# Performance work log

Measured on AMD Instinct MI355X. Metric: run time of the kernel, lower is better.

## Reference

```python
import jax, jax.numpy as jnp
import numpy as np

B, T, D = 4, 2048, 1024
H = 16
HD = D // H

def setup_inputs() -> dict:
    key = jax.random.key(0)
    k1, k2, k3, k4, k5 = jax.random.split(key, 5)
    x = jax.random.normal(k1, (B, T, D), dtype=jnp.float32)
    scale = 1.0 / np.sqrt(D)
    W_qkv = jax.random.normal(k2, (D, 3 * D), dtype=jnp.float32) * scale
    b_qkv = jnp.zeros((3 * D,), dtype=jnp.float32)
    W_proj = jax.random.normal(k3, (D, D), dtype=jnp.float32) * scale
    b_proj = jnp.zeros((D,), dtype=jnp.float32)
    return {"x": x, "W_qkv": W_qkv, "b_qkv": b_qkv, "W_proj": W_proj, "b_proj": b_proj}

def reference(x, W_qkv, b_qkv, W_proj, b_proj):
    Bx, Tx, C = x.shape
    qkv = x @ W_qkv + b_qkv                      # [B,T,3C]
    q, k, v = jnp.split(qkv, 3, axis=-1)
    # [B,T,H,hd] -> [B,H,T,hd]
    q = q.reshape(Bx, Tx, H, HD).transpose(0, 2, 1, 3)
    k = k.reshape(Bx, Tx, H, HD).transpose(0, 2, 1, 3)
    v = v.reshape(Bx, Tx, H, HD).transpose(0, 2, 1, 3)
    att = jnp.einsum('bhqd,bhkd->bhqk', q, k) / jnp.sqrt(jnp.float32(HD))
    causal = jnp.tril(jnp.ones((Tx, Tx), dtype=bool))
    att = jnp.where(causal[None, None], att, -jnp.inf)
    att = jax.nn.softmax(att, axis=-1)
    y = jnp.einsum('bhqk,bhkd->bhqd', att, v)    # [B,H,T,hd]
    y = y.transpose(0, 2, 1, 3).reshape(Bx, Tx, C)
    return y @ W_proj + b_proj
```

## Files before the change

### kernel.cpp

```cpp
#include <hip/hip_runtime.h>
#include <hip/hip_bf16.h>

#define B_  4
#define T_  2048
#define D_  1024
#define H_  16
#define HD_ 64

typedef short s16x8 __attribute__((ext_vector_type(8)));
typedef short s16x4 __attribute__((ext_vector_type(4)));
typedef float f32x4 __attribute__((ext_vector_type(4)));
typedef unsigned int u32x2 __attribute__((ext_vector_type(2)));

#define MFMA32(a, b, c) __builtin_amdgcn_mfma_f32_16x16x32_bf16(a, b, c, 0, 0, 0)
#define MFMA16(a, b, c) __builtin_amdgcn_mfma_f32_16x16x16bf16_1k(a, b, c, 0, 0, 0)

__device__ __forceinline__ unsigned short f2bf(float f) {
  unsigned u = __builtin_bit_cast(unsigned, f);
  u += 0x7fffu + ((u >> 16) & 1u);
  return (unsigned short)(u >> 16);
}

__device__ __forceinline__ float bf2f(unsigned short h) {
  return __builtin_bit_cast(float, (unsigned)h << 16);
}

#define GLOAD_LDS16(src, dst)                                            \
  __builtin_amdgcn_global_load_lds(                                      \
      (__attribute__((address_space(1))) void*)(void*)(src),             \
      (__attribute__((address_space(3))) void*)(dst), 16, 0, 0)

__global__ __launch_bounds__(256) void convert_x_kernel(
    const float* __restrict__ in, unsigned short* __restrict__ out, int n8) {
  int i = blockIdx.x * 256 + threadIdx.x;
  if (i >= n8) return;
  const float4* p = ((const float4*)in) + (size_t)i * 2;
  float4 a = p[0], b = p[1];
  s16x8 o;
  o[0] = (short)f2bf(a.x); o[1] = (short)f2bf(a.y);
  o[2] = (short)f2bf(a.z); o[3] = (short)f2bf(a.w);
  o[4] = (short)f2bf(b.x); o[5] = (short)f2bf(b.y);
  o[6] = (short)f2bf(b.z); o[7] = (short)f2bf(b.w);
  *(((s16x8*)out) + i) = o;
}

__global__ __launch_bounds__(256) void transpose_w_kernel(
    const float* __restrict__ W, unsigned short* __restrict__ Wt, int K, int N) {
  __shared__ float tile[32][33];
  int n0 = blockIdx.x * 32, k0 = blockIdx.y * 32;
  int tx = threadIdx.x & 31, ty = threadIdx.x >> 5;
#pragma unroll
  for (int j = 0; j < 4; ++j) {
    int k = ty + j * 8;
    tile[k][tx] = W[(size_t)(k0 + k) * N + n0 + tx];
  }
  __syncthreads();
#pragma unroll
  for (int j = 0; j < 4; ++j) {
    int n = ty + j * 8;
    Wt[(size_t)(n0 + n) * K + k0 + tx] = f2bf(tile[tx][n]);
  }
}

template <int OUTF32>
__global__ __launch_bounds__(256) void gemm_kernel(
    const unsigned short* __restrict__ A, const unsigned short* __restrict__ Bt,
    const float* __restrict__ bias, void* __restrict__ Cout, int M, int N, int K) {
  __shared__ char lds[32768];
  char* Al = lds;
  char* Bl = lds + 16384;
  const int n0 = blockIdx.x * 128, m0 = blockIdx.y * 128;
  const int w = threadIdx.x >> 6, lane = threadIdx.x & 63;
  const int l15 = lane & 15, g = lane >> 4;
  const int wr = w >> 1, wc = w & 1;
  const int srow = (lane >> 3);
  const int u = lane & 7;
  const int soct = (u ^ srow) << 3;
  const int rx = l15 & 7;
  f32x4 acc[4][4] = {};

  for (int kt = 0; kt < K; kt += 64) {
    __syncthreads();
#pragma unroll
    for (int i = 0; i < 4; ++i) {
      int c = w * 4 + i;
      int row = c * 8 + srow;
      const unsigned short* srcA = A + (size_t)(m0 + row) * K + kt + soct;
      GLOAD_LDS16(srcA, Al + c * 1024);
      const unsigned short* srcB = Bt + (size_t)(n0 + row) * K + kt + soct;
      GLOAD_LDS16(srcB, Bl + c * 1024);
    }
    __syncthreads();
#pragma unroll
    for (int kk = 0; kk < 2; ++kk) {
      const int roct = ((kk * 4 + g) ^ rx) << 4;
      s16x8 af[4], bfr[4];
#pragma unroll
      for (int mi = 0; mi < 4; ++mi) {
        int row = wr * 64 + mi * 16 + l15;
        af[mi] = *(const s16x8*)(Al + row * 128 + roct);
      }
#pragma unroll
      for (int ni = 0; ni < 4; ++ni) {
        int row = wc * 64 + ni * 16 + l15;
        bfr[ni] = *(const s16x8*)(Bl + row * 128 + roct);
      }
#pragma unroll
      for (int mi = 0; mi < 4; ++mi)
#pragma unroll
        for (int ni = 0; ni < 4; ++ni)
          acc[mi][ni] = MFMA32(af[mi], bfr[ni], acc[mi][ni]);
    }
  }
#pragma unroll
  for (int ni = 0; ni < 4; ++ni) {
    int col = n0 + wc * 64 + ni * 16 + l15;
    float bv = bias[col];
#pragma unroll
    for (int mi = 0; mi < 4; ++mi) {
      int row = m0 + wr * 64 + mi * 16 + g * 4;
#pragma unroll
      for (int r = 0; r < 4; ++r) {
        float v = acc[mi][ni][r] + bv;
        if (OUTF32)
          ((float*)Cout)[(size_t)(row + r) * N + col] = v;
        else
          ((unsigned short*)Cout)[(size_t)(row + r) * N + col] = f2bf(v);
      }
    }
  }
}

#define VT_STR 76
#define VT_BLK 1232
__global__ __launch_bounds__(256, 2) void attn_kernel(
    const unsigned short* __restrict__ qkv, unsigned short* __restrict__ yatt) {
  __shared__ char lds[18048];
  const int bx = blockIdx.x;
  const int bh = blockIdx.y;
  const int b = bh >> 4, h = bh & 15;
  const int w = threadIdx.x >> 6;
  const int lane = threadIdx.x & 63;
  const int l15 = lane & 15, g = lane >> 4;

  const size_t rowstride = 3 * D_;
  const unsigned short* Qb = qkv + (size_t)b * T_ * rowstride + h * HD_;
  const unsigned short* Kb = Qb + D_;
  const unsigned short* Vb = Qb + 2 * D_;

  char* Klds = lds;
  unsigned short* Vt = (unsigned short*)(lds + 8192);

  const int krow0 = (w * 2 + 0) * 8 + (lane >> 3);
  const int krow1 = (w * 2 + 1) * 8 + (lane >> 3);
  const int u = lane & 7;
  const int vkey = w * 16 + (lane >> 2);
  const int vdb = lane & 3;
  const float SC = 0.18033688011112042f;
  const s16x4 onesf = {(short)0x3F80, (short)0x3F80, (short)0x3F80, (short)0x3F80};

  const int qtA_t = 15 - bx;
  const int nA = 2 * qtA_t + 2;

  s16x8 kc0, kc1, vc0, vc1;
  s16x8 kn0, kn1, vn0, vn1;

  auto ld = [&](int kt, s16x8& a, s16x8& b2, s16x8& c, s16x8& d2) {
    const unsigned short* kb = Kb + (size_t)(kt * 64) * rowstride;
    a = *(const s16x8*)(kb + (size_t)krow0 * rowstride + u * 8);
    b2 = *(const s16x8*)(kb + (size_t)krow1 * rowstride + u * 8);
    const unsigned short* vs = Vb + (size_t)(kt * 64 + vkey) * rowstride + vdb * 16;
    c = *(const s16x8*)(vs);
    d2 = *(const s16x8*)(vs + 8);
  };

  ld(0, kc0, kc1, vc0, vc1);
  ld(1, kn0, kn1, vn0, vn1);
  int f = 0;

#pragma unroll 1
  for (int ti = 0; ti < 2; ++ti) {
    const int qt = ti ? bx : qtA_t;
    const int ntk = 2 * qt + 2;
    const int base = qt * 128 + w * 32;
    s16x8 qfA0, qfA1, qfB0, qfB1;
    {
      const unsigned short* qa = Qb + (size_t)(base + l15) * rowstride;
      const unsigned short* qb = Qb + (size_t)(base + 16 + l15) * rowstride;
      s16x8 a0 = *(const s16x8*)(qa + g * 8);
      s16x8 a1 = *(const s16x8*)(qa + 32 + g * 8);
      s16x8 b0 = *(const s16x8*)(qb + g * 8);
      s16x8 b1 = *(const s16x8*)(qb + 32 + g * 8);
#pragma unroll
      for (int j = 0; j < 8; ++j) {
        qfA0[j] = (short)f2bf(bf2f((unsigned short)a0[j]) * SC);
        qfA1[j] = (short)f2bf(bf2f((unsigned short)a1[j]) * SC);
        qfB0[j] = (short)f2bf(bf2f((unsigned short)b0[j]) * SC);
        qfB1[j] = (short)f2bf(bf2f((unsigned short)b1[j]) * SC);
      }
    }
    float mA = -1e30f, mB = -1e30f;
    f32x4 accA[4] = {}, accB[4] = {};
    f32x4 accSA = {}, accSB = {};

#pragma unroll 1
    for (int kt = 0; kt < ntk; ++kt) {
      __syncthreads();
      *(s16x8*)(Klds + krow0 * 128 + ((u ^ (krow0 & 7)) << 4)) = kc0;
      *(s16x8*)(Klds + krow1 * 128 + ((u ^ (krow1 & 7)) << 4)) = kc1;
#pragma unroll
      for (int j = 0; j < 8; ++j) {
        Vt[vdb * VT_BLK + j * VT_STR + vkey] = (unsigned short)vc0[j];
        Vt[vdb * VT_BLK + (8 + j) * VT_STR + vkey] = (unsigned short)vc1[j];
      }
      __syncthreads();
      kc0 = kn0; kc1 = kn1; vc0 = vn0; vc1 = vn1;
      {
        int f2 = f + 2;
        if (f2 < 34) {
          int kt2 = (f2 < nA) ? f2 : f2 - nA;
          ld(kt2, kn0, kn1, vn0, vn1);
        }
      }
      ++f;

      if (kt * 64 > base + 31) continue;

      float tvA[16], tvB[16];
      __builtin_amdgcn_s_setprio(1);
#pragma unroll
      for (int kk = 0; kk < 4; ++kk) {
        int key = kk * 16 + l15;
        const s16x8 kf0 = *(const s16x8*)(Klds + key * 128 + ((g ^ (key & 7)) << 4));
        const s16x8 kf1 = *(const s16x8*)(Klds + key * 128 + (((4 + g) ^ (key & 7)) << 4));
        f32x4 sA = {}, sB = {};
        sA = MFMA32(kf0, qfA0, sA);
        sA = MFMA32(kf1, qfA1, sA);
        sB = MFMA32(kf0, qfB0, sB);
        sB = MFMA32(kf1, qfB1, sB);
#pragma unroll
        for (int r = 0; r < 4; ++r) { tvA[kk * 4 + r] = sA[r]; tvB[kk * 4 + r] = sB[r]; }
      }
      __builtin_amdgcn_s_setprio(0);
      if (kt * 64 + 63 > base) {
        int qA = base + l15, qB = base + 16 + l15;
#pragma unroll
        for (int kk = 0; kk < 4; ++kk)
#pragma unroll
          for (int r = 0; r < 4; ++r) {
            int key = kt * 64 + kk * 16 + g * 4 + r;
            if (key > qA) tvA[kk * 4 + r] = -1e30f;
            if (key > qB) tvB[kk * 4 + r] = -1e30f;
          }
      }
      s16x4 pbA[4], pbB[4];
      {
        float a0 = fmaxf(fmaxf(tvA[0], tvA[1]), tvA[2]);
        float a1 = fmaxf(fmaxf(tvA[3], tvA[4]), tvA[5]);
        float a2 = fmaxf(fmaxf(tvA[6], tvA[7]), tvA[8]);
        float a3 = fmaxf(fmaxf(tvA[9], tvA[10]), tvA[11]);
        float a4 = fmaxf(fmaxf(tvA[12], tvA[13]), tvA[14]);
        float tm = fmaxf(fmaxf(fmaxf(a0, a1), a2), fmaxf(fmaxf(a3, a4), tvA[15]));
        tm = fmaxf(tm, __shfl_xor(tm, 16));
        tm = fmaxf(tm, __shfl_xor(tm, 32));
        if (!__all(tm - mA <= 8.0f)) {
          float mn = fmaxf(mA, tm);
          float corr = exp2f(mA - mn);
          mA = mn;
#pragma unroll
          for (int i = 0; i < 4; ++i) {
            accA[i][0] *= corr; accA[i][1] *= corr;
            accA[i][2] *= corr; accA[i][3] *= corr;
          }
          accSA[0] *= corr; accSA[1] *= corr; accSA[2] *= corr; accSA[3] *= corr;
        }
#pragma unroll
        for (int kk = 0; kk < 4; ++kk) {
          float p0 = exp2f(tvA[kk * 4 + 0] - mA), p1 = exp2f(tvA[kk * 4 + 1] - mA);
          float p2 = exp2f(tvA[kk * 4 + 2] - mA), p3 = exp2f(tvA[kk * 4 + 3] - mA);
          u32x2 pk;
          pk[0] = __builtin_amdgcn_perm(__builtin_bit_cast(unsigned, p1),
                                        __builtin_bit_cast(unsigned, p0), 0x07060302u);
          pk[1] = __builtin_amdgcn_perm(__builtin_bit_cast(unsigned, p3),
                                        __builtin_bit_cast(unsigned, p2), 0x07060302u);
          pbA[kk] = __builtin_bit_cast(s16x4, pk);
        }
      }
      {
        float a0 = fmaxf(fmaxf(tvB[0], tvB[1]), tvB[2]);
        float a1 = fmaxf(fmaxf(tvB[3], tvB[4]), tvB[5]);
        float a2 = fmaxf(fmaxf(tvB[6], tvB[7]), tvB[8]);
        float a3 = fmaxf(fmaxf(tvB[9], tvB[10]), tvB[11]);
        float a4 = fmaxf(fmaxf(tvB[12], tvB[13]), tvB[14]);
        float tm = fmaxf(fmaxf(fmaxf(a0, a1), a2), fmaxf(fmaxf(a3, a4), tvB[15]));
        tm = fmaxf(tm, __shfl_xor(tm, 16));
        tm = fmaxf(tm, __shfl_xor(tm, 32));
        if (!__all(tm - mB <= 8.0f)) {
          float mn = fmaxf(mB, tm);
          float corr = exp2f(mB - mn);
          mB = mn;
#pragma unroll
          for (int i = 0; i < 4; ++i) {
            accB[i][0] *= corr; accB[i][1] *= corr;
            accB[i][2] *= corr; accB[i][3] *= corr;
          }
          accSB[0] *= corr; accSB[1] *= corr; accSB[2] *= corr; accSB[3] *= corr;
        }
#pragma unroll
        for (int kk = 0; kk < 4; ++kk) {
          float p0 = exp2f(tvB[kk * 4 + 0] - mB), p1 = exp2f(tvB[kk * 4 + 1] - mB);
          float p2 = exp2f(tvB[kk * 4 + 2] - mB), p3 = exp2f(tvB[kk * 4 + 3] - mB);
          u32x2 pk;
          pk[0] = __builtin_amdgcn_perm(__builtin_bit_cast(unsigned, p1),
                                        __builtin_bit_cast(unsigned, p0), 0x07060302u);
          pk[1] = __builtin_amdgcn_perm(__builtin_bit_cast(unsigned, p3),
                                        __builtin_bit_cast(unsigned, p2), 0x07060302u);
          pbB[kk] = __builtin_bit_cast(s16x4, pk);
        }
      }
      __builtin_amdgcn_s_setprio(1);
#pragma unroll
      for (int kk = 0; kk < 4; ++kk) {
#pragma unroll
        for (int db = 0; db < 4; ++db) {
          s16x4 vf = *(const s16x4*)(Vt + db * VT_BLK + l15 * VT_STR + kk * 16 + g * 4);
          accA[db] = MFMA16(vf, pbA[kk], accA[db]);
          accB[db] = MFMA16(vf, pbB[kk], accB[db]);
        }
        accSA = MFMA16(onesf, pbA[kk], accSA);
        accSB = MFMA16(onesf, pbB[kk], accSB);
      }
      __builtin_amdgcn_s_setprio(0);
    }

    float invA = 1.0f / accSA[0];
    float invB = 1.0f / accSB[0];
    __syncthreads();
    unsigned short* ylds = (unsigned short*)lds;
#pragma unroll
    for (int db = 0; db < 4; ++db)
#pragma unroll
      for (int r = 0; r < 4; ++r) {
        int d = db * 16 + g * 4 + r;
        ylds[d * 130 + w * 32 + l15] = f2bf(accA[db][r] * invA);
        ylds[d * 130 + w * 32 + 16 + l15] = f2bf(accB[db][r] * invB);
      }
    __syncthreads();
    {
      int qq = threadIdx.x >> 1;
      int dc = (threadIdx.x & 1) * 32;
      s16x8 o0, o1, o2, o3;
#pragma unroll
      for (int j = 0; j < 8; ++j) {
        o0[j] = (short)ylds[(dc + j) * 130 + qq];
        o1[j] = (short)ylds[(dc + 8 + j) * 130 + qq];
        o2[j] = (short)ylds[(dc + 16 + j) * 130 + qq];
        o3[j] = (short)ylds[(dc + 24 + j) * 130 + qq];
      }
      unsigned short* dst =
          yatt + (size_t)(b * T_ + qt * 128 + qq) * D_ + h * HD_ + dc;
      *(s16x8*)(dst) = o0;
      *(s16x8*)(dst + 8) = o1;
      *(s16x8*)(dst + 16) = o2;
      *(s16x8*)(dst + 24) = o3;
    }
  }
}

extern "C" void kernel_launch(void* const* d_in, const int* in_sizes, int n_in,
                              void* d_out, int out_size, void* d_ws, size_t ws_size,
                              hipStream_t stream) {
  const float* x     = (const float*)d_in[0];
  const float* Wqkv  = (const float*)d_in[1];
  const float* bqkv  = (const float*)d_in[2];
  const float* Wproj = (const float*)d_in[3];
  const float* bproj = (const float*)d_in[4];
  float* out = (float*)d_out;

  unsigned short* xb   = (unsigned short*)d_ws;
  unsigned short* Wqb  = xb + (size_t)8192 * 1024;
  unsigned short* Wpb  = Wqb + (size_t)3072 * 1024;
  unsigned short* qkvb = Wpb + (size_t)1024 * 1024;
  unsigned short* yb   = xb;

  convert_x_kernel<<<dim3(4096), dim3(256), 0, stream>>>(x, xb, 8192 * 1024 / 8);
  transpose_w_kernel<<<dim3(96, 32), dim3(256), 0, stream>>>(Wqkv, Wqb, 1024, 3072);
  transpose_w_kernel<<<dim3(32, 32), dim3(256), 0, stream>>>(Wproj, Wpb, 1024, 1024);
  gemm_kernel<0><<<dim3(24, 64), dim3(256), 0, stream>>>(xb, Wqb, bqkv, qkvb, 8192, 3072, 1024);
  attn_kernel<<<dim3(8, 64), dim3(256), 0, stream>>>(qkvb, yb);
  gemm_kernel<1><<<dim3(8, 64), dim3(256), 0, stream>>>(yb, Wpb, bproj, out, 8192, 1024, 1024);
}
```

Measured before the change: 193.2 us.

## Double-buffer GEMM LDS loads and split attention into one query tile per block

After: 185.1 us. 4.2% less time.

```diff
diff --git a/kernel.cpp b/kernel.cpp
--- a/kernel.cpp
+++ b/kernel.cpp
@@ -63,12 +63,10 @@
 }
 
 template <int OUTF32>
-__global__ __launch_bounds__(256) void gemm_kernel(
+__global__ __launch_bounds__(256, 2) void gemm_kernel(
     const unsigned short* __restrict__ A, const unsigned short* __restrict__ Bt,
     const float* __restrict__ bias, void* __restrict__ Cout, int M, int N, int K) {
-  __shared__ char lds[32768];
-  char* Al = lds;
-  char* Bl = lds + 16384;
+  __shared__ char lds[65536];
   const int n0 = blockIdx.x * 128, m0 = blockIdx.y * 128;
   const int w = threadIdx.x >> 6, lane = threadIdx.x & 63;
   const int l15 = lane & 15, g = lane >> 4;
@@ -79,18 +77,34 @@
   const int rx = l15 & 7;
   f32x4 acc[4][4] = {};
 
-  for (int kt = 0; kt < K; kt += 64) {
-    __syncthreads();
+  auto stage = [&](int buf, int kt) {
+    char* Ab = lds + buf * 32768;
+    char* Bb = Ab + 16384;
 #pragma unroll
     for (int i = 0; i < 4; ++i) {
       int c = w * 4 + i;
       int row = c * 8 + srow;
-      const unsigned short* srcA = A + (size_t)(m0 + row) * K + kt + soct;
-      GLOAD_LDS16(srcA, Al + c * 1024);
-      const unsigned short* srcB = Bt + (size_t)(n0 + row) * K + kt + soct;
-      GLOAD_LDS16(srcB, Bl + c * 1024);
-    }
-    __syncthreads();
+      GLOAD_LDS16(A + (size_t)(m0 + row) * K + kt + soct, Ab + c * 1024);
+      GLOAD_LDS16(Bt + (size_t)(n0 + row) * K + kt + soct, Bb + c * 1024);
+    }
+  };
+
+  stage(0, 0);
+  __syncthreads();
+  int cur = 0;
+
+  for (int kt = 0; kt < K; kt += 64) {
+    __builtin_amdgcn_s_barrier();
+    if (kt + 64 < K) {
+      stage(cur ^ 1, kt + 64);
+      asm volatile("s_waitcnt vmcnt(8)" ::: "memory");
+    } else {
+      asm volatile("s_waitcnt vmcnt(0)" ::: "memory");
+    }
+    __builtin_amdgcn_s_barrier();
+    __builtin_amdgcn_sched_barrier(0);
+    const char* Al = lds + cur * 32768;
+    const char* Bl = Al + 16384;
 #pragma unroll
     for (int kk = 0; kk < 2; ++kk) {
       const int roct = ((kk * 4 + g) ^ rx) << 4;
@@ -111,6 +125,7 @@
         for (int ni = 0; ni < 4; ++ni)
           acc[mi][ni] = MFMA32(af[mi], bfr[ni], acc[mi][ni]);
     }
+    cur ^= 1;
   }
 #pragma unroll
   for (int ni = 0; ni < 4; ++ni) {
@@ -133,11 +148,11 @@
 
 #define VT_STR 76
 #define VT_BLK 1232
-__global__ __launch_bounds__(256, 2) void attn_kernel(
+__global__ __launch_bounds__(256, 4) void attn_kernel(
     const unsigned short* __restrict__ qkv, unsigned short* __restrict__ yatt) {
-  __shared__ char lds[18048];
-  const int bx = blockIdx.x;
-  const int bh = blockIdx.y;
+  __shared__ char lds[8192 + 4 * VT_BLK * 2];
+  const int bh = blockIdx.x;
+  const int qt = 15 - blockIdx.y;
   const int b = bh >> 4, h = bh & 15;
   const int w = threadIdx.x >> 6;
   const int lane = threadIdx.x & 63;
@@ -159,211 +174,193 @@
   const float SC = 0.18033688011112042f;
   const s16x4 onesf = {(short)0x3F80, (short)0x3F80, (short)0x3F80, (short)0x3F80};
 
-  const int qtA_t = 15 - bx;
-  const int nA = 2 * qtA_t + 2;
-
-  s16x8 kc0, kc1, vc0, vc1;
-  s16x8 kn0, kn1, vn0, vn1;
-
-  auto ld = [&](int kt, s16x8& a, s16x8& b2, s16x8& c, s16x8& d2) {
+  s16x8 kreg0, kreg1, vreg0, vreg1;
+  auto ld = [&](int kt) {
     const unsigned short* kb = Kb + (size_t)(kt * 64) * rowstride;
-    a = *(const s16x8*)(kb + (size_t)krow0 * rowstride + u * 8);
-    b2 = *(const s16x8*)(kb + (size_t)krow1 * rowstride + u * 8);
+    kreg0 = *(const s16x8*)(kb + (size_t)krow0 * rowstride + u * 8);
+    kreg1 = *(const s16x8*)(kb + (size_t)krow1 * rowstride + u * 8);
     const unsigned short* vs = Vb + (size_t)(kt * 64 + vkey) * rowstride + vdb * 16;
-    c = *(const s16x8*)(vs);
-    d2 = *(const s16x8*)(vs + 8);
+    vreg0 = *(const s16x8*)(vs);
+    vreg1 = *(const s16x8*)(vs + 8);
   };
 
-  ld(0, kc0, kc1, vc0, vc1);
-  ld(1, kn0, kn1, vn0, vn1);
-  int f = 0;
+  const int base = qt * 128 + w * 32;
+  const int ntk = 2 * qt + 2;
+
+  s16x8 qfA0, qfA1, qfB0, qfB1;
+  {
+    const unsigned short* qa = Qb + (size_t)(base + l15) * rowstride;
+    const unsigned short* qb = Qb + (size_t)(base + 16 + l15) * rowstride;
+    s16x8 a0 = *(const s16x8*)(qa + g * 8);
+    s16x8 a1 = *(const s16x8*)(qa + 32 + g * 8);
+    s16x8 b0 = *(const s16x8*)(qb + g * 8);
+    s16x8 b1 = *(const s16x8*)(qb + 32 + g * 8);
+#pragma unroll
+    for (int j = 0; j < 8; ++j) {
+      qfA0[j] = (short)f2bf(bf2f((unsigned short)a0[j]) * SC);
+      qfA1[j] = (short)f2bf(bf2f((unsigned short)a1[j]) * SC);
+      qfB0[j] = (short)f2bf(bf2f((unsigned short)b0[j]) * SC);
+      qfB1[j] = (short)f2bf(bf2f((unsigned short)b1[j]) * SC);
+    }
+  }
+
+  ld(0);
+  float mA = -1e30f, mB = -1e30f;
+  f32x4 accA[4] = {}, accB[4] = {};
+  f32x4 accSA = {}, accSB = {};
 
 #pragma unroll 1
-  for (int ti = 0; ti < 2; ++ti) {
-    const int qt = ti ? bx : qtA_t;
-    const int ntk = 2 * qt + 2;
-    const int base = qt * 128 + w * 32;
-    s16x8 qfA0, qfA1, qfB0, qfB1;
+  for (int kt = 0; kt < ntk; ++kt) {
+    __syncthreads();
+    *(s16x8*)(Klds + krow0 * 128 + ((u ^ (krow0 & 7)) << 4)) = kreg0;
+    *(s16x8*)(Klds + krow1 * 128 + ((u ^ (krow1 & 7)) << 4)) = kreg1;
+#pragma unroll
+    for (int j = 0; j < 8; ++j) {
+      Vt[vdb * VT_BLK + j * VT_STR + vkey] = (unsigned short)vreg0[j];
+      Vt[vdb * VT_BLK + (8 + j) * VT_STR + vkey] = (unsigned short)vreg1[j];
+    }
+    __syncthreads();
+    if (kt < ntk - 1) ld(kt + 1);
+
+    if (kt * 64 > base + 31) continue;
+
+    float tvA[16], tvB[16];
+    __builtin_amdgcn_s_setprio(1);
+#pragma unroll
+    for (int kk = 0; kk < 4; ++kk) {
+      int key = kk * 16 + l15;
+      const s16x8 kf0 = *(const s16x8*)(Klds + key * 128 + ((g ^ (key & 7)) << 4));
+      const s16x8 kf1 = *(const s16x8*)(Klds + key * 128 + (((4 + g) ^ (key & 7)) << 4));
+      f32x4 sA = {}, sB = {};
+      sA = MFMA32(kf0, qfA0, sA);
+      sA = MFMA32(kf1, qfA1, sA);
+      sB = MFMA32(kf0, qfB0, sB);
+      sB = MFMA32(kf1, qfB1, sB);
+#pragma unroll
+      for (int r = 0; r < 4; ++r) { tvA[kk * 4 + r] = sA[r]; tvB[kk * 4 + r] = sB[r]; }
+    }
+    __builtin_amdgcn_s_setprio(0);
+    if (kt * 64 + 63 > base) {
+      int qA = base + l15, qB = base + 16 + l15;
+#pragma unroll
+      for (int kk = 0; kk < 4; ++kk)
+#pragma unroll
+        for (int r = 0; r < 4; ++r) {
+          int key = kt * 64 + kk * 16 + g * 4 + r;
+          if (key > qA) tvA[kk * 4 + r] = -1e30f;
+          if (key > qB) tvB[kk * 4 + r] = -1e30f;
+        }
+    }
+    s16x4 pbA[4], pbB[4];
     {
-      const unsigned short* qa = Qb + (size_t)(base + l15) * rowstride;
-      const unsigned short* qb = Qb + (size_t)(base + 16 + l15) * rowstride;
-      s16x8 a0 = *(const s16x8*)(qa + g * 8);
-      s16x8 a1 = *(const s16x8*)(qa + 32 + g * 8);
-      s16x8 b0 = *(const s16x8*)(qb + g * 8);
-      s16x8 b1 = *(const s16x8*)(qb + 32 + g * 8);
-#pragma unroll
-      for (int j = 0; j < 8; ++j) {
-        qfA0[j] = (short)f2bf(bf2f((unsigned short)a0[j]) * SC);
-        qfA1[j] = (short)f2bf(bf2f((unsigned short)a1[j]) * SC);
-        qfB0[j] = (short)f2bf(bf2f((unsigned short)b0[j]) * SC);
-        qfB1[j] = (short)f2bf(bf2f((unsigned short)b1[j]) * SC);
-      }
-    }
-    float mA = -1e30f, mB = -1e30f;
-    f32x4 accA[4] = {}, accB[4] = {};
-    f32x4 accSA = {}, accSB = {};
-
-#pragma unroll 1
-    for (int kt = 0; kt < ntk; ++kt) {
-      __syncthreads();
-      *(s16x8*)(Klds + krow0 * 128 + ((u ^ (krow0 & 7)) << 4)) = kc0;
-      *(s16x8*)(Klds + krow1 * 128 + ((u ^ (krow1 & 7)) << 4)) = kc1;
-#pragma unroll
-      for (int j = 0; j < 8; ++j) {
-        Vt[vdb * VT_BLK + j * VT_STR + vkey] = (unsigned short)vc0[j];
-        Vt[vdb * VT_BLK + (8 + j) * VT_STR + vkey] = (unsigned short)vc1[j];
-      }
-      __syncthreads();
-      kc0 = kn0; kc1 = kn1; vc0 = vn0; vc1 = vn1;
-      {
-        int f2 = f + 2;
-        if (f2 < 34) {
-          int kt2 = (f2 < nA) ? f2 : f2 - nA;
-          ld(kt2, kn0, kn1, vn0, vn1);
+      float a0 = fmaxf(fmaxf(tvA[0], tvA[1]), tvA[2]);
+      float a1 = fmaxf(fmaxf(tvA[3], tvA[4]), tvA[5]);
+      float a2 = fmaxf(fmaxf(tvA[6], tvA[7]), tvA[8]);
+      float a3 = fmaxf(fmaxf(tvA[9], tvA[10]), tvA[11]);
+      float a4 = fmaxf(fmaxf(tvA[12], tvA[13]), tvA[14]);
+      float tm = fmaxf(fmaxf(fmaxf(a0, a1), a2), fmaxf(fmaxf(a3, a4), tvA[15]));
+      tm = fmaxf(tm, __shfl_xor(tm, 16));
+      tm = fmaxf(tm, __shfl_xor(tm, 32));
+      if (!__all(tm - mA <= 8.0f)) {
+        float mn = fmaxf(mA, tm);
+        float corr = exp2f(mA - mn);
+        mA = mn;
+#pragma unroll
+        for (int i = 0; i < 4; ++i) {
+          accA[i][0] *= corr; accA[i][1] *= corr;
+          accA[i][2] *= corr; accA[i][3] *= corr;
         }
-      }
-      ++f;
-
-      if (kt * 64 > base + 31) continue;
-
-      float tvA[16], tvB[16];
-      __builtin_amdgcn_s_setprio(1);
+        accSA[0] *= corr; accSA[1] *= corr; accSA[2] *= corr; accSA[3] *= corr;
+      }
 #pragma unroll
       for (int kk = 0; kk < 4; ++kk) {
-        int key = kk * 16 + l15;
-        const s16x8 kf0 = *(const s16x8*)(Klds + key * 128 + ((g ^ (key & 7)) << 4));
-        const s16x8 kf1 = *(const s16x8*)(Klds + key * 128 + (((4 + g) ^ (key & 7)) << 4));
-        f32x4 sA = {}, sB = {};
-        sA = MFMA32(kf0, qfA0, sA);
-        sA = MFMA32(kf1, qfA1, sA);
-        sB = MFMA32(kf0, qfB0, sB);
-        sB = MFMA32(kf1, qfB1, sB);
-#pragma unroll
-        for (int r = 0; r < 4; ++r) { tvA[kk * 4 + r] = sA[r]; tvB[kk * 4 + r] = sB[r]; }
-      }
-      __builtin_amdgcn_s_setprio(0);
-      if (kt * 64 + 63 > base) {
-        int qA = base + l15, qB = base + 16 + l15;
-#pragma unroll
-        for (int kk = 0; kk < 4; ++kk)
-#pragma unroll
-          for (int r = 0; r < 4; ++r) {
-            int key = kt * 64 + kk * 16 + g * 4 + r;
-            if (key > qA) tvA[kk * 4 + r] = -1e30f;
-            if (key > qB) tvB[kk * 4 + r] = -1e30f;
-          }
-      }
-      s16x4 pbA[4], pbB[4];
-      {
-        float a0 = fmaxf(fmaxf(tvA[0], tvA[1]), tvA[2]);
-        float a1 = fmaxf(fmaxf(tvA[3], tvA[4]), tvA[5]);
-        float a2 = fmaxf(fmaxf(tvA[6], tvA[7]), tvA[8]);
-        float a3 = fmaxf(fmaxf(tvA[9], tvA[10]), tvA[11]);
-        float a4 = fmaxf(fmaxf(tvA[12], tvA[13]), tvA[14]);
-        float tm = fmaxf(fmaxf(fmaxf(a0, a1), a2), fmaxf(fmaxf(a3, a4), tvA[15]));
-        tm = fmaxf(tm, __shfl_xor(tm, 16));
-        tm = fmaxf(tm, __shfl_xor(tm, 32));
-        if (!__all(tm - mA <= 8.0f)) {
-          float mn = fmaxf(mA, tm);
-          float corr = exp2f(mA - mn);
-          mA = mn;
-#pragma unroll
-          for (int i = 0; i < 4; ++i) {
-            accA[i][0] *= corr; accA[i][1] *= corr;
-            accA[i][2] *= corr; accA[i][3] *= corr;
-          }
-          accSA[0] *= corr; accSA[1] *= corr; accSA[2] *= corr; accSA[3] *= corr;
+        float p0 = exp2f(tvA[kk * 4 + 0] - mA), p1 = exp2f(tvA[kk * 4 + 1] - mA);
+        float p2 = exp2f(tvA[kk * 4 + 2] - mA), p3 = exp2f(tvA[kk * 4 + 3] - mA);
+        u32x2 pk;
+        pk[0] = __builtin_amdgcn_perm(__builtin_bit_cast(unsigned, p1),
+                                      __builtin_bit_cast(unsigned, p0), 0x07060302u);
+        pk[1] = __builtin_amdgcn_perm(__builtin_bit_cast(unsigned, p3),
+                                      __builtin_bit_cast(unsigned, p2), 0x07060302u);
+        pbA[kk] = __builtin_bit_cast(s16x4, pk);
+      }
+    }
+    {
+      float a0 = fmaxf(fmaxf(tvB[0], tvB[1]), tvB[2]);
+      float a1 = fmaxf(fmaxf(tvB[3], tvB[4]), tvB[5]);
+      float a2 = fmaxf(fmaxf(tvB[6], tvB[7]), tvB[8]);
+      float a3 = fmaxf(fmaxf(tvB[9], tvB[10]), tvB[11]);
+      float a4 = fmaxf(fmaxf(tvB[12], tvB[13]), tvB[14]);
+      float tm = fmaxf(fmaxf(fmaxf(a0, a1), a2), fmaxf(fmaxf(a3, a4), tvB[15]));
+      tm = fmaxf(tm, __shfl_xor(tm, 16));
+      tm = fmaxf(tm, __shfl_xor(tm, 32));
+      if (!__all(tm - mB <= 8.0f)) {
+        float mn = fmaxf(mB, tm);
+        float corr = exp2f(mB - mn);
+        mB = mn;
+#pragma unroll
+        for (int i = 0; i < 4; ++i) {
+          accB[i][0] *= corr; accB[i][1] *= corr;
+          accB[i][2] *= corr; accB[i][3] *= corr;
         }
-#pragma unroll
-        for (int kk = 0; kk < 4; ++kk) {
-          float p0 = exp2f(tvA[kk * 4 + 0] - mA), p1 = exp2f(tvA[kk * 4 + 1] - mA);
-          float p2 = exp2f(tvA[kk * 4 + 2] - mA), p3 = exp2f(tvA[kk * 4 + 3] - mA);
-          u32x2 pk;
-          pk[0] = __builtin_amdgcn_perm(__builtin_bit_cast(unsigned, p1),
-                                        __builtin_bit_cast(unsigned, p0), 0x07060302u);
-          pk[1] = __builtin_amdgcn_perm(__builtin_bit_cast(unsigned, p3),
-                                        __builtin_bit_cast(unsigned, p2), 0x07060302u);
-          pbA[kk] = __builtin_bit_cast(s16x4, pk);
-        }
-      }
-      {
-        float a0 = fmaxf(fmaxf(tvB[0], tvB[1]), tvB[2]);
-        float a1 = fmaxf(fmaxf(tvB[3], tvB[4]), tvB[5]);
-        float a2 = fmaxf(fmaxf(tvB[6], tvB[7]), tvB[8]);
-        float a3 = fmaxf(fmaxf(tvB[9], tvB[10]), tvB[11]);
-        float a4 = fmaxf(fmaxf(tvB[12], tvB[13]), tvB[14]);
-        float tm = fmaxf(fmaxf(fmaxf(a0, a1), a2), fmaxf(fmaxf(a3, a4), tvB[15]));
-        tm = fmaxf(tm, __shfl_xor(tm, 16));
-        tm = fmaxf(tm, __shfl_xor(tm, 32));
-        if (!__all(tm - mB <= 8.0f)) {
-          float mn = fmaxf(mB, tm);
-          float corr = exp2f(mB - mn);
-          mB = mn;
-#pragma unroll
-          for (int i = 0; i < 4; ++i) {
-            accB[i][0] *= corr; accB[i][1] *= corr;
-            accB[i][2] *= corr; accB[i][3] *= corr;
-          }
-          accSB[0] *= corr; accSB[1] *= corr; accSB[2] *= corr; accSB[3] *= corr;
-        }
-#pragma unroll
-        for (int kk = 0; kk < 4; ++kk) {
-          float p0 = exp2f(tvB[kk * 4 + 0] - mB), p1 = exp2f(tvB[kk * 4 + 1] - mB);
-          float p2 = exp2f(tvB[kk * 4 + 2] - mB), p3 = exp2f(tvB[kk * 4 + 3] - mB);
-          u32x2 pk;
-          pk[0] = __builtin_amdgcn_perm(__builtin_bit_cast(unsigned, p1),
-                                        __builtin_bit_cast(unsigned, p0), 0x07060302u);
-          pk[1] = __builtin_amdgcn_perm(__builtin_bit_cast(unsigned, p3),
-                                        __builtin_bit_cast(unsigned, p2), 0x07060302u);
-          pbB[kk] = __builtin_bit_cast(s16x4, pk);
-        }
-      }
-      __builtin_amdgcn_s_setprio(1);
+        accSB[0] *= corr; accSB[1] *= corr; accSB[2] *= corr; accSB[3] *= corr;
+      }
 #pragma unroll
       for (int kk = 0; kk < 4; ++kk) {
-#pragma unroll
-        for (int db = 0; db < 4; ++db) {
-          s16x4 vf = *(const s16x4*)(Vt + db * VT_BLK + l15 * VT_STR + kk * 16 + g * 4);
-          accA[db] = MFMA16(vf, pbA[kk], accA[db]);
-          accB[db] = MFMA16(vf, pbB[kk], accB[db]);
-        }
-        accSA = MFMA16(onesf, pbA[kk], accSA);
-        accSB = MFMA16(onesf, pbB[kk], accSB);
-      }
-      __builtin_amdgcn_s_setprio(0);
-    }
-
-    float invA = 1.0f / accSA[0];
-    float invB = 1.0f / accSB[0];
-    __syncthreads();
-    unsigned short* ylds = (unsigned short*)lds;
-#pragma unroll
-    for (int db = 0; db < 4; ++db)
-#pragma unroll
-      for (int r = 0; r < 4; ++r) {
-        int d = db * 16 + g * 4 + r;
-        ylds[d * 130 + w * 32 + l15] = f2bf(accA[db][r] * invA);
-        ylds[d * 130 + w * 32 + 16 + l15] = f2bf(accB[db][r] * invB);
-      }
-    __syncthreads();
-    {
-      int qq = threadIdx.x >> 1;
-      int dc = (threadIdx.x & 1) * 32;
-      s16x8 o0, o1, o2, o3;
-#pragma unroll
-      for (int j = 0; j < 8; ++j) {
-        o0[j] = (short)ylds[(dc + j) * 130 + qq];
-        o1[j] = (short)ylds[(dc + 8 + j) * 130 + qq];
-        o2[j] = (short)ylds[(dc + 16 + j) * 130 + qq];
-        o3[j] = (short)ylds[(dc + 24 + j) * 130 + qq];
-      }
-      unsigned short* dst =
-          yatt + (size_t)(b * T_ + qt * 128 + qq) * D_ + h * HD_ + dc;
-      *(s16x8*)(dst) = o0;
-      *(s16x8*)(dst + 8) = o1;
-      *(s16x8*)(dst + 16) = o2;
-      *(s16x8*)(dst + 24) = o3;
-    }
+        float p0 = exp2f(tvB[kk * 4 + 0] - mB), p1 = exp2f(tvB[kk * 4 + 1] - mB);
+        float p2 = exp2f(tvB[kk * 4 + 2] - mB), p3 = exp2f(tvB[kk * 4 + 3] - mB);
+        u32x2 pk;
+        pk[0] = __builtin_amdgcn_perm(__builtin_bit_cast(unsigned, p1),
+                                      __builtin_bit_cast(unsigned, p0), 0x07060302u);
+        pk[1] = __builtin_amdgcn_perm(__builtin_bit_cast(unsigned, p3),
+                                      __builtin_bit_cast(unsigned, p2), 0x07060302u);
+        pbB[kk] = __builtin_bit_cast(s16x4, pk);
+      }
+    }
+    __builtin_amdgcn_s_setprio(1);
+#pragma unroll
+    for (int kk = 0; kk < 4; ++kk) {
+#pragma unroll
+      for (int db = 0; db < 4; ++db) {
+        s16x4 vf = *(const s16x4*)(Vt + db * VT_BLK + l15 * VT_STR + kk * 16 + g * 4);
+        accA[db] = MFMA16(vf, pbA[kk], accA[db]);
+        accB[db] = MFMA16(vf, pbB[kk], accB[db]);
+      }
+      accSA = MFMA16(onesf, pbA[kk], accSA);
+      accSB = MFMA16(onesf, pbB[kk], accSB);
+    }
+    __builtin_amdgcn_s_setprio(0);
+  }
+
+  float invA = 1.0f / accSA[0];
+  float invB = 1.0f / accSB[0];
+  __syncthreads();
+  unsigned short* ylds = (unsigned short*)lds;
+#pragma unroll
+  for (int db = 0; db < 4; ++db)
+#pragma unroll
+    for (int r = 0; r < 4; ++r) {
+      int d = db * 16 + g * 4 + r;
+      ylds[d * 130 + w * 32 + l15] = f2bf(accA[db][r] * invA);
+      ylds[d * 130 + w * 32 + 16 + l15] = f2bf(accB[db][r] * invB);
+    }
+  __syncthreads();
+  {
+    int qq = threadIdx.x >> 1;
+    int dc = (threadIdx.x & 1) * 32;
+    s16x8 o0, o1, o2, o3;
+#pragma unroll
+    for (int j = 0; j < 8; ++j) {
+      o0[j] = (short)ylds[(dc + j) * 130 + qq];
+      o1[j] = (short)ylds[(dc + 8 + j) * 130 + qq];
+      o2[j] = (short)ylds[(dc + 16 + j) * 130 + qq];
+      o3[j] = (short)ylds[(dc + 24 + j) * 130 + qq];
+    }
+    unsigned short* dst =
+        yatt + (size_t)(b * T_ + qt * 128 + qq) * D_ + h * HD_ + dc;
+    *(s16x8*)(dst) = o0;
+    *(s16x8*)(dst + 8) = o1;
+    *(s16x8*)(dst + 16) = o2;
+    *(s16x8*)(dst + 24) = o3;
   }
 }
 
@@ -387,6 +384,6 @@
   transpose_w_kernel<<<dim3(96, 32), dim3(256), 0, stream>>>(Wqkv, Wqb, 1024, 3072);
   transpose_w_kernel<<<dim3(32, 32), dim3(256), 0, stream>>>(Wproj, Wpb, 1024, 1024);
   gemm_kernel<0><<<dim3(24, 64), dim3(256), 0, stream>>>(xb, Wqb, bqkv, qkvb, 8192, 3072, 1024);
-  attn_kernel<<<dim3(8, 64), dim3(256), 0, stream>>>(qkvb, yb);
+  attn_kernel<<<dim3(64, 16), dim3(256), 0, stream>>>(qkvb, yb);
   gemm_kernel<1><<<dim3(8, 64), dim3(256), 0, stream>>>(yb, Wpb, bproj, out, 8192, 1024, 1024);
 }
```
